# Kernel tuning notes

Hardware: AMD Instinct MI355X
Metric: run time of the kernel (lower is better)

## Reference

```python
import jax, jax.numpy as jnp
import numpy as np

H = 32  # hidden_size
NUM_LAYERS = 3
INPUT_SIZE = 64
STD = 0.1


def setup_inputs() -> dict:
    key = jax.random.key(0)
    ks = jax.random.split(key, 2 * NUM_LAYERS + 2)
    inp = {}
    inp["x"] = jax.random.normal(ks[0], (256, 2048, INPUT_SIZE), dtype=jnp.float32)
    in_dim = INPUT_SIZE
    for l in range(NUM_LAYERS):
        inp[f"W_ih{l}"] = STD * jax.random.normal(ks[1 + 2 * l], (4 * H, in_dim), dtype=jnp.float32)
        inp[f"W_hh{l}"] = STD * jax.random.normal(ks[2 + 2 * l], (4 * H, H), dtype=jnp.float32)
        inp[f"b{l}"] = jnp.zeros((4 * H,), dtype=jnp.float32)  # b_ih + b_hh, both init to 0
        in_dim = H
    inp["W_out"] = STD * jax.random.normal(ks[-1], (1, H), dtype=jnp.float32)
    inp["b_out"] = jnp.zeros((1,), dtype=jnp.float32)
    return inp


def _lstm_layer(x, W_ih, W_hh, b):
    # x: [B, T, D_in] -> h_seq: [B, T, H]
    B = x.shape[0]
    # precompute input-to-gate projections for all timesteps (one big GEMM)
    xg = jnp.einsum('btd,gd->btg', x, W_ih) + b          # [B, T, 4H]
    xg = jnp.swapaxes(xg, 0, 1)                           # [T, B, 4H]
    W_hh_T = W_hh.T                                       # [H, 4H]

    def step(carry, xg_t):
        h, c = carry
        g = xg_t + h @ W_hh_T                             # [B, 4H]
        i = jax.nn.sigmoid(g[:, 0 * H:1 * H])
        f = jax.nn.sigmoid(g[:, 1 * H:2 * H])
        gg = jnp.tanh(g[:, 2 * H:3 * H])
        o = jax.nn.sigmoid(g[:, 3 * H:4 * H])
        c = f * c + i * gg
        h = o * jnp.tanh(c)
        return (h, c), h

    h0 = jnp.zeros((B, H), dtype=x.dtype)
    c0 = jnp.zeros((B, H), dtype=x.dtype)
    _, h_seq = jax.lax.scan(step, (h0, c0), xg)           # h_seq: [T, B, H]
    return jnp.swapaxes(h_seq, 0, 1)                      # [B, T, H]


def reference(x, W_ih0, W_hh0, b0, W_ih1, W_hh1, b1, W_ih2, W_hh2, b2, W_out, b_out):
    h = _lstm_layer(x, W_ih0, W_hh0, b0)
    h = _lstm_layer(h, W_ih1, W_hh1, b1)
    h = _lstm_layer(h, W_ih2, W_hh2, b2)
    last = h[:, -1, :]                                    # [B, H]
    return last @ W_out.T + b_out                         # [B, 1]
```

## Files before the change

kernel.cpp:

```cpp
#include <hip/hip_runtime.h>


typedef float v2f __attribute__((ext_vector_type(2)));

constexpr int T_SEQ  = 2048;
constexpr int CH     = 16;
constexpr int NCHUNK = T_SEQ / CH;
constexpr int NPHASE = NCHUNK + 5;

#define GLOAD_LDS16(gsrc, ldst)                                                              \
    __builtin_amdgcn_global_load_lds((const __attribute__((address_space(1))) void*)(gsrc), \
                                     (__attribute__((address_space(3))) void*)(ldst),        \
                                     16, 0, 0)
#define KEEPV(x) asm volatile("" : "+v"(x))

__device__ __forceinline__ float rcp_f(float x) { return __builtin_amdgcn_rcpf(x); }

__device__ __forceinline__ float swap_sum32(float x) {
#if __has_builtin(__builtin_amdgcn_permlane32_swap)
    auto r = __builtin_amdgcn_permlane32_swap(__float_as_uint(x), __float_as_uint(x),
                                              false, false);
    return __uint_as_float(r[0]) + __uint_as_float(r[1]);
#else
    return x + __shfl_xor(x, 32);
#endif
}

template<bool RING>
__device__ __forceinline__ void rec_chunk(int l,
    const v2f* __restrict__ xg_in,
    float* __restrict__ ring_out,
    const v2f (&whA)[16], const v2f (&whB)[16],
    float (&hs)[32], float& c, float& z,
    float mt, float ca, float cb)
{
    v2f xgr[CH];
#pragma unroll
    for (int tt = 0; tt < CH; ++tt) xgr[tt] = xg_in[tt * 64 + l];

#pragma unroll
    for (int tt = 0; tt < CH; ++tt) {
        v2f aA0 = {xgr[tt].x, 0.f}, aA1 = {0.f, 0.f};
        v2f aB0 = {xgr[tt].y, 0.f}, aB1 = {0.f, 0.f};
#pragma unroll
        for (int j = 0; j < 16; j += 2) {
            const v2f h0 = {hs[2*j],     hs[2*j + 1]};
            const v2f h1 = {hs[2*j + 2], hs[2*j + 3]};
            aA0 = h0 * whA[j]     + aA0;
            aB0 = h0 * whB[j]     + aB0;
            aA1 = h1 * whA[j + 1] + aA1;
            aB1 = h1 * whB[j + 1] + aB1;
        }
        const float ga = (aA0.x + aA1.x) + (aA0.y + aA1.y);
        const float gb = (aB0.x + aB1.x) + (aB0.y + aB1.y);

        const float sA = rcp_f(1.0f + __expf(-ga));
        const float eb = __expf(mt * gb);
        const float tb = fmaf(-2.0f, rcp_f(eb + 1.0f), 1.0f);
        const float vB = fmaf(ca, tb, cb);

        const float p  = sA * ((l < 32) ? vB : c);
        const float cn = swap_sum32(p);
        const float ec = __expf(2.0f * cn);
        const float th = fmaf(-2.0f, rcp_f(ec + 1.0f), 1.0f);
        z = vB * th;
        c = cn;

        if constexpr (RING) { if (l >= 32) ring_out[tt * 32 + (l - 32)] = z; }

        const int zb = __float_as_int(z);
#pragma unroll
        for (int k = 0; k < 32; ++k)
            hs[k] = __int_as_float(__builtin_amdgcn_readlane(zb, k + 32));
    }
}

__device__ __forceinline__ void feed_h_chunk(int l, const float* __restrict__ hr,
    v2f* __restrict__ xg_out, const v2f (&wA)[16], const v2f (&wB)[16],
    float bA, float bB)
{
#pragma unroll
    for (int tt = 0; tt < CH; ++tt) {
        const float4* h4 = reinterpret_cast<const float4*>(hr + tt * 32);
        v2f a0 = {bA, 0.f}, a1 = {0.f, 0.f}, b0 = {bB, 0.f}, b1 = {0.f, 0.f};
#pragma unroll
        for (int i = 0; i < 8; ++i) {
            const float4 v = h4[i];
            const v2f lo = {v.x, v.y}, hi = {v.z, v.w};
            a0 = lo * wA[2*i] + a0;  a1 = hi * wA[2*i+1] + a1;
            b0 = lo * wB[2*i] + b0;  b1 = hi * wB[2*i+1] + b1;
        }
        xg_out[tt * 64 + l] = (v2f){(a0.x + a1.x) + (a0.y + a1.y),
                                    (b0.x + b1.x) + (b0.y + b1.y)};
    }
}

__device__ __forceinline__ void feed0_chunk(int l, const float* __restrict__ xs,
    v2f* __restrict__ xg_out, const v2f (&wA)[32], const v2f (&wB)[32],
    float bA, float bB)
{
#pragma unroll
    for (int tt = 0; tt < CH; ++tt) {
        const float4* xt = reinterpret_cast<const float4*>(xs + tt * 64);
        v2f a0 = {bA, 0.f}, a1 = {0.f, 0.f}, b0 = {bB, 0.f}, b1 = {0.f, 0.f};
#pragma unroll
        for (int i = 0; i < 16; ++i) {
            const float4 v = xt[i];
            const v2f lo = {v.x, v.y}, hi = {v.z, v.w};
            a0 = lo * wA[2*i] + a0;  a1 = hi * wA[2*i+1] + a1;
            b0 = lo * wB[2*i] + b0;  b1 = hi * wB[2*i+1] + b1;
        }
        xg_out[tt * 64 + l] = (v2f){(a0.x + a1.x) + (a0.y + a1.y),
                                    (b0.x + b1.x) + (b0.y + b1.y)};
    }
}

__global__ __launch_bounds__(512, 1)
void lstm3_iso_kernel(const float* __restrict__ x,
    const float* __restrict__ W_ih0, const float* __restrict__ W_hh0, const float* __restrict__ b0,
    const float* __restrict__ W_ih1, const float* __restrict__ W_hh1, const float* __restrict__ b1,
    const float* __restrict__ W_ih2, const float* __restrict__ W_hh2, const float* __restrict__ b2,
    const float* __restrict__ W_out, const float* __restrict__ b_out,
    float* __restrict__ out)
{
    const int bi = blockIdx.x;
    const int w  = threadIdx.x >> 6;
    const int l  = threadIdx.x & 63;

    __shared__ v2f   xg0[2][CH][64];
    __shared__ v2f   xg1[2][CH][64];
    __shared__ v2f   xg2[2][CH][64];
    __shared__ float h0r[2][CH][32];
    __shared__ float h1r[2][CH][32];
    __shared__ float xstage[2][CH * 64];

    if (w == 0) {
        __builtin_amdgcn_s_setprio(1);
        v2f whA[16], whB[16];
        const v2f* hA = reinterpret_cast<const v2f*>(W_hh0 + l * 32);
        const v2f* hB = reinterpret_cast<const v2f*>(W_hh0 + (l + 64) * 32);
#pragma unroll
        for (int i = 0; i < 16; ++i) { whA[i] = hA[i]; KEEPV(whA[i]); whB[i] = hB[i]; KEEPV(whB[i]); }
        const float mt = (l < 32) ? 2.f : 1.f;
        const float ca = (l < 32) ? 1.f : 0.5f;
        const float cb = (l < 32) ? 0.f : 0.5f;
        float hs[32];
#pragma unroll
        for (int k = 0; k < 32; ++k) hs[k] = 0.f;
        float c = 0.f, z = 0.f;
        __syncthreads();
        for (int p = 0; p < NPHASE; ++p) {
            const int ci = p - 1;
            if (ci >= 0 && ci < NCHUNK)
                rec_chunk<true>(l, &xg0[ci & 1][0][0], &h0r[ci & 1][0][0],
                                whA, whB, hs, c, z, mt, ca, cb);
            __syncthreads();
        }
    } else if (w == 1) {
        __builtin_amdgcn_s_setprio(1);
        v2f whA[16], whB[16];
        const v2f* hA = reinterpret_cast<const v2f*>(W_hh1 + l * 32);
        const v2f* hB = reinterpret_cast<const v2f*>(W_hh1 + (l + 64) * 32);
#pragma unroll
        for (int i = 0; i < 16; ++i) { whA[i] = hA[i]; KEEPV(whA[i]); whB[i] = hB[i]; KEEPV(whB[i]); }
        const float mt = (l < 32) ? 2.f : 1.f;
        const float ca = (l < 32) ? 1.f : 0.5f;
        const float cb = (l < 32) ? 0.f : 0.5f;
        float hs[32];
#pragma unroll
        for (int k = 0; k < 32; ++k) hs[k] = 0.f;
        float c = 0.f, z = 0.f;
        __syncthreads();
        for (int p = 0; p < NPHASE; ++p) {
            const int ci = p - 3;
            if (ci >= 0 && ci < NCHUNK)
                rec_chunk<true>(l, &xg1[ci & 1][0][0], &h1r[ci & 1][0][0],
                                whA, whB, hs, c, z, mt, ca, cb);
            __syncthreads();
        }
    } else if (w == 2) {
        __builtin_amdgcn_s_setprio(1);
        v2f whA[16], whB[16];
        const v2f* hA = reinterpret_cast<const v2f*>(W_hh2 + l * 32);
        const v2f* hB = reinterpret_cast<const v2f*>(W_hh2 + (l + 64) * 32);
#pragma unroll
        for (int i = 0; i < 16; ++i) { whA[i] = hA[i]; KEEPV(whA[i]); whB[i] = hB[i]; KEEPV(whB[i]); }
        const float mt = (l < 32) ? 2.f : 1.f;
        const float ca = (l < 32) ? 1.f : 0.5f;
        const float cb = (l < 32) ? 0.f : 0.5f;
        const float woutv = W_out[l & 31];
        float hs[32];
#pragma unroll
        for (int k = 0; k < 32; ++k) hs[k] = 0.f;
        float c = 0.f, z = 0.f;
        __syncthreads();
        for (int p = 0; p < NPHASE; ++p) {
            const int ci = p - 5;
            if (ci >= 0 && ci < NCHUNK)
                rec_chunk<false>(l, &xg2[ci & 1][0][0], nullptr,
                                 whA, whB, hs, c, z, mt, ca, cb);
            __syncthreads();
        }
        float s = (l >= 32) ? z * woutv : 0.f;
#pragma unroll
        for (int off = 32; off; off >>= 1) s += __shfl_xor(s, off);
        if (l == 0) out[bi] = s + b_out[0];
    } else if (w == 3) {
        v2f wA[32], wB[32];
        const v2f* pA = reinterpret_cast<const v2f*>(W_ih0 + l * 64);
        const v2f* pB = reinterpret_cast<const v2f*>(W_ih0 + (l + 64) * 64);
#pragma unroll
        for (int i = 0; i < 32; ++i) { wA[i] = pA[i]; KEEPV(wA[i]); wB[i] = pB[i]; KEEPV(wB[i]); }
        const float bAv = b0[l], bBv = b0[l + 64];
        const float* src = x + (size_t)bi * T_SEQ * 64;
#pragma unroll
        for (int i = 0; i < 4; ++i)
            GLOAD_LDS16(src + i * 256 + l * 4, &xstage[0][i * 256 + l * 4]);
        __syncthreads();
        for (int p = 0; p < NPHASE; ++p) {
            if (p + 1 < NCHUNK) {
                const float* ns = src + (size_t)(p + 1) * CH * 64;
                float* dst = &xstage[(p + 1) & 1][0];
#pragma unroll
                for (int i = 0; i < 4; ++i)
                    GLOAD_LDS16(ns + i * 256 + l * 4, dst + i * 256 + l * 4);
            }
            if (p < NCHUNK)
                feed0_chunk(l, xstage[p & 1], &xg0[p & 1][0][0], wA, wB, bAv, bBv);
            __syncthreads();
        }
    } else if (w == 7) {
        v2f w1A[16], w1B[16], w2A[16], w2B[16];
        const v2f* p1A = reinterpret_cast<const v2f*>(W_ih1 + l * 32);
        const v2f* p1B = reinterpret_cast<const v2f*>(W_ih1 + (l + 64) * 32);
        const v2f* p2A = reinterpret_cast<const v2f*>(W_ih2 + l * 32);
        const v2f* p2B = reinterpret_cast<const v2f*>(W_ih2 + (l + 64) * 32);
#pragma unroll
        for (int i = 0; i < 16; ++i) {
            w1A[i] = p1A[i]; KEEPV(w1A[i]); w1B[i] = p1B[i]; KEEPV(w1B[i]);
            w2A[i] = p2A[i]; KEEPV(w2A[i]); w2B[i] = p2B[i]; KEEPV(w2B[i]);
        }
        const float b1A = b1[l], b1B = b1[l + 64];
        const float b2A = b2[l], b2B = b2[l + 64];
        __syncthreads();
        for (int p = 0; p < NPHASE; ++p) {
            const int c1 = p - 2;
            if (c1 >= 0 && c1 < NCHUNK)
                feed_h_chunk(l, &h0r[c1 & 1][0][0], &xg1[c1 & 1][0][0], w1A, w1B, b1A, b1B);
            const int c2 = p - 4;
            if (c2 >= 0 && c2 < NCHUNK)
                feed_h_chunk(l, &h1r[c2 & 1][0][0], &xg2[c2 & 1][0][0], w2A, w2B, b2A, b2B);
            __syncthreads();
        }
    } else {
        __syncthreads();
        for (int p = 0; p < NPHASE; ++p) __syncthreads();
    }
}

extern "C" void kernel_launch(void* const* d_in, const int* in_sizes, int n_in,
                              void* d_out, int out_size, void* d_ws, size_t ws_size,
                              hipStream_t stream) {
    const float* x      = (const float*)d_in[0];
    const float* W_ih0  = (const float*)d_in[1];
    const float* W_hh0  = (const float*)d_in[2];
    const float* b0     = (const float*)d_in[3];
    const float* W_ih1  = (const float*)d_in[4];
    const float* W_hh1  = (const float*)d_in[5];
    const float* b1     = (const float*)d_in[6];
    const float* W_ih2  = (const float*)d_in[7];
    const float* W_hh2  = (const float*)d_in[8];
    const float* b2     = (const float*)d_in[9];
    const float* W_out  = (const float*)d_in[10];
    const float* b_out  = (const float*)d_in[11];

    lstm3_iso_kernel<<<256, 512, 0, stream>>>(x,
                                              W_ih0, W_hh0, b0,
                                              W_ih1, W_hh1, b1,
                                              W_ih2, W_hh2, b2,
                                              W_out, b_out,
                                              (float*)d_out);
}
```

Measured before the change: 802.5 us.

## Interleave two batch sequences per wave to hide recurrent step latency

Each block now processes two batch elements, and each recurrent wave interleaves the time steps of the two independent sequences so one sequence's latency chain can overlap the other's. The hidden-state broadcast moves from 32 readlanes to an LDS write plus float4 reads. The idle waves 4–7 now split the layer-1/2 input projections by half-chunk. The grid halves to 128 blocks, so fewer CUs are used in exchange for more instruction-level parallelism per wave, and the LDS round trip adds latency to each step.

```diff
diff --git a/kernel.cpp b/kernel.cpp
--- a/kernel.cpp
+++ b/kernel.cpp
@@ -26,61 +26,74 @@
 #endif
 }
 
+__device__ __forceinline__ void rec_step(int l, v2f xgv,
+    const v2f (&whA)[16], const v2f (&whB)[16],
+    const float4 (&hv)[8], float& c, float& z,
+    float mt, float ca, float cb)
+{
+    v2f aA0 = {xgv.x, 0.f}, aA1 = {0.f, 0.f};
+    v2f aB0 = {xgv.y, 0.f}, aB1 = {0.f, 0.f};
+#pragma unroll
+    for (int i = 0; i < 8; ++i) {
+        const v2f lo = {hv[i].x, hv[i].y}, hi = {hv[i].z, hv[i].w};
+        aA0 = lo * whA[2*i]   + aA0;  aA1 = hi * whA[2*i+1] + aA1;
+        aB0 = lo * whB[2*i]   + aB0;  aB1 = hi * whB[2*i+1] + aB1;
+    }
+    const float ga = (aA0.x + aA1.x) + (aA0.y + aA1.y);
+    const float gb = (aB0.x + aB1.x) + (aB0.y + aB1.y);
+
+    const float sA = rcp_f(1.0f + __expf(-ga));
+    const float eb = __expf(mt * gb);
+    const float tb = fmaf(-2.0f, rcp_f(eb + 1.0f), 1.0f);
+    const float vB = fmaf(ca, tb, cb);
+
+    const float p  = sA * ((l < 32) ? vB : c);
+    const float cn = swap_sum32(p);
+    const float ec = __expf(2.0f * cn);
+    const float th = fmaf(-2.0f, rcp_f(ec + 1.0f), 1.0f);
+    z = vB * th;
+    c = cn;
+}
+
 template<bool RING>
-__device__ __forceinline__ void rec_chunk(int l,
-    const v2f* __restrict__ xg_in,
-    float* __restrict__ ring_out,
+__device__ __forceinline__ void rec_chunk2(int l,
+    const v2f* __restrict__ xgA, const v2f* __restrict__ xgB,
+    float* __restrict__ ringA, float* __restrict__ ringB,
+    float* hbA, float* hbB,
     const v2f (&whA)[16], const v2f (&whB)[16],
-    float (&hs)[32], float& c, float& z,
+    float4 (&hvA)[8], float4 (&hvB)[8],
+    float& cA, float& zA, float& cB, float& zB,
     float mt, float ca, float cb)
 {
-    v2f xgr[CH];
-#pragma unroll
-    for (int tt = 0; tt < CH; ++tt) xgr[tt] = xg_in[tt * 64 + l];
-
+    v2f xa = xgA[l], xb = xgB[l];
 #pragma unroll
     for (int tt = 0; tt < CH; ++tt) {
-        v2f aA0 = {xgr[tt].x, 0.f}, aA1 = {0.f, 0.f};
-        v2f aB0 = {xgr[tt].y, 0.f}, aB1 = {0.f, 0.f};
-#pragma unroll
-        for (int j = 0; j < 16; j += 2) {
-            const v2f h0 = {hs[2*j],     hs[2*j + 1]};
-            const v2f h1 = {hs[2*j + 2], hs[2*j + 3]};
-            aA0 = h0 * whA[j]     + aA0;
-            aB0 = h0 * whB[j]     + aB0;
-            aA1 = h1 * whA[j + 1] + aA1;
-            aB1 = h1 * whB[j + 1] + aB1;
-        }
-        const float ga = (aA0.x + aA1.x) + (aA0.y + aA1.y);
-        const float gb = (aB0.x + aB1.x) + (aB0.y + aB1.y);
-
-        const float sA = rcp_f(1.0f + __expf(-ga));
-        const float eb = __expf(mt * gb);
-        const float tb = fmaf(-2.0f, rcp_f(eb + 1.0f), 1.0f);
-        const float vB = fmaf(ca, tb, cb);
-
-        const float p  = sA * ((l < 32) ? vB : c);
-        const float cn = swap_sum32(p);
-        const float ec = __expf(2.0f * cn);
-        const float th = fmaf(-2.0f, rcp_f(ec + 1.0f), 1.0f);
-        z = vB * th;
-        c = cn;
-
-        if constexpr (RING) { if (l >= 32) ring_out[tt * 32 + (l - 32)] = z; }
-
-        const int zb = __float_as_int(z);
-#pragma unroll
-        for (int k = 0; k < 32; ++k)
-            hs[k] = __int_as_float(__builtin_amdgcn_readlane(zb, k + 32));
-    }
-}
-
-__device__ __forceinline__ void feed_h_chunk(int l, const float* __restrict__ hr,
+        rec_step(l, xa, whA, whB, hvA, cA, zA, mt, ca, cb);
+        hbA[l] = zA;
+        if constexpr (RING) { if (l >= 32) ringA[tt*32 + (l-32)] = zA; }
+        {   const float4* h4 = reinterpret_cast<const float4*>(hbA + 32);
+#pragma unroll
+            for (int i = 0; i < 8; ++i) hvA[i] = h4[i];
+        }
+        if (tt + 1 < CH) xa = xgA[(tt+1)*64 + l];
+        rec_step(l, xb, whA, whB, hvB, cB, zB, mt, ca, cb);
+        hbB[l] = zB;
+        if constexpr (RING) { if (l >= 32) ringB[tt*32 + (l-32)] = zB; }
+        {   const float4* h4 = reinterpret_cast<const float4*>(hbB + 32);
+#pragma unroll
+            for (int i = 0; i < 8; ++i) hvB[i] = h4[i];
+        }
+        if (tt + 1 < CH) xb = xgB[(tt+1)*64 + l];
+    }
+}
+
+__device__ __forceinline__ void feed_h_half(int l, const float* __restrict__ hr,
     v2f* __restrict__ xg_out, const v2f (&wA)[16], const v2f (&wB)[16],
-    float bA, float bB)
-{
-#pragma unroll
-    for (int tt = 0; tt < CH; ++tt) {
+    float bA, float bB, int tt0)
+{
+#pragma unroll
+    for (int t = 0; t < CH/2; ++t) {
+        const int tt = tt0 + t;
         const float4* h4 = reinterpret_cast<const float4*>(hr + tt * 32);
         v2f a0 = {bA, 0.f}, a1 = {0.f, 0.f}, b0 = {bB, 0.f}, b1 = {0.f, 0.f};
 #pragma unroll
@@ -116,7 +129,7 @@
 }
 
 __global__ __launch_bounds__(512, 1)
-void lstm3_iso_kernel(const float* __restrict__ x,
+void lstm3_dual_kernel(const float* __restrict__ x,
     const float* __restrict__ W_ih0, const float* __restrict__ W_hh0, const float* __restrict__ b0,
     const float* __restrict__ W_ih1, const float* __restrict__ W_hh1, const float* __restrict__ b1,
     const float* __restrict__ W_ih2, const float* __restrict__ W_hh2, const float* __restrict__ b2,
@@ -127,84 +140,53 @@
     const int w  = threadIdx.x >> 6;
     const int l  = threadIdx.x & 63;
 
-    __shared__ v2f   xg0[2][CH][64];
-    __shared__ v2f   xg1[2][CH][64];
-    __shared__ v2f   xg2[2][CH][64];
-    __shared__ float h0r[2][CH][32];
-    __shared__ float h1r[2][CH][32];
-    __shared__ float xstage[2][CH * 64];
-
-    if (w == 0) {
+    __shared__ v2f   xg[3][2][2][CH][64];
+    __shared__ float ring[2][2][2][CH][32];
+    __shared__ float xstage[2][2][CH * 64];
+    __shared__ float hbuf[3][2][64];
+
+    if (w == 0 || w == 1 || w == 2) {
+        const int L = w;
         __builtin_amdgcn_s_setprio(1);
+        const float* Whh = (L == 0) ? W_hh0 : (L == 1) ? W_hh1 : W_hh2;
         v2f whA[16], whB[16];
-        const v2f* hA = reinterpret_cast<const v2f*>(W_hh0 + l * 32);
-        const v2f* hB = reinterpret_cast<const v2f*>(W_hh0 + (l + 64) * 32);
-#pragma unroll
-        for (int i = 0; i < 16; ++i) { whA[i] = hA[i]; KEEPV(whA[i]); whB[i] = hB[i]; KEEPV(whB[i]); }
-        const float mt = (l < 32) ? 2.f : 1.f;
-        const float ca = (l < 32) ? 1.f : 0.5f;
-        const float cb = (l < 32) ? 0.f : 0.5f;
-        float hs[32];
-#pragma unroll
-        for (int k = 0; k < 32; ++k) hs[k] = 0.f;
-        float c = 0.f, z = 0.f;
-        __syncthreads();
-        for (int p = 0; p < NPHASE; ++p) {
-            const int ci = p - 1;
-            if (ci >= 0 && ci < NCHUNK)
-                rec_chunk<true>(l, &xg0[ci & 1][0][0], &h0r[ci & 1][0][0],
-                                whA, whB, hs, c, z, mt, ca, cb);
-            __syncthreads();
-        }
-    } else if (w == 1) {
-        __builtin_amdgcn_s_setprio(1);
-        v2f whA[16], whB[16];
-        const v2f* hA = reinterpret_cast<const v2f*>(W_hh1 + l * 32);
-        const v2f* hB = reinterpret_cast<const v2f*>(W_hh1 + (l + 64) * 32);
-#pragma unroll
-        for (int i = 0; i < 16; ++i) { whA[i] = hA[i]; KEEPV(whA[i]); whB[i] = hB[i]; KEEPV(whB[i]); }
-        const float mt = (l < 32) ? 2.f : 1.f;
-        const float ca = (l < 32) ? 1.f : 0.5f;
-        const float cb = (l < 32) ? 0.f : 0.5f;
-        float hs[32];
-#pragma unroll
-        for (int k = 0; k < 32; ++k) hs[k] = 0.f;
-        float c = 0.f, z = 0.f;
-        __syncthreads();
-        for (int p = 0; p < NPHASE; ++p) {
-            const int ci = p - 3;
-            if (ci >= 0 && ci < NCHUNK)
-                rec_chunk<true>(l, &xg1[ci & 1][0][0], &h1r[ci & 1][0][0],
-                                whA, whB, hs, c, z, mt, ca, cb);
-            __syncthreads();
-        }
-    } else if (w == 2) {
-        __builtin_amdgcn_s_setprio(1);
-        v2f whA[16], whB[16];
-        const v2f* hA = reinterpret_cast<const v2f*>(W_hh2 + l * 32);
-        const v2f* hB = reinterpret_cast<const v2f*>(W_hh2 + (l + 64) * 32);
+        const v2f* hA = reinterpret_cast<const v2f*>(Whh + l * 32);
+        const v2f* hB = reinterpret_cast<const v2f*>(Whh + (l + 64) * 32);
 #pragma unroll
         for (int i = 0; i < 16; ++i) { whA[i] = hA[i]; KEEPV(whA[i]); whB[i] = hB[i]; KEEPV(whB[i]); }
         const float mt = (l < 32) ? 2.f : 1.f;
         const float ca = (l < 32) ? 1.f : 0.5f;
         const float cb = (l < 32) ? 0.f : 0.5f;
         const float woutv = W_out[l & 31];
-        float hs[32];
-#pragma unroll
-        for (int k = 0; k < 32; ++k) hs[k] = 0.f;
-        float c = 0.f, z = 0.f;
+        float4 hvA[8], hvB[8];
+#pragma unroll
+        for (int i = 0; i < 8; ++i) { hvA[i] = make_float4(0.f,0.f,0.f,0.f); hvB[i] = hvA[i]; }
+        float cA = 0.f, zA = 0.f, cB = 0.f, zB = 0.f;
+        const int skew = 2 * L + 1;
         __syncthreads();
         for (int p = 0; p < NPHASE; ++p) {
-            const int ci = p - 5;
-            if (ci >= 0 && ci < NCHUNK)
-                rec_chunk<false>(l, &xg2[ci & 1][0][0], nullptr,
-                                 whA, whB, hs, c, z, mt, ca, cb);
+            const int ci = p - skew;
+            if (ci >= 0 && ci < NCHUNK) {
+                if (L < 2)
+                    rec_chunk2<true>(l, &xg[L][0][ci&1][0][0], &xg[L][1][ci&1][0][0],
+                                     &ring[L][0][ci&1][0][0], &ring[L][1][ci&1][0][0],
+                                     hbuf[L][0], hbuf[L][1],
+                                     whA, whB, hvA, hvB, cA, zA, cB, zB, mt, ca, cb);
+                else
+                    rec_chunk2<false>(l, &xg[2][0][ci&1][0][0], &xg[2][1][ci&1][0][0],
+                                      nullptr, nullptr,
+                                      hbuf[2][0], hbuf[2][1],
+                                      whA, whB, hvA, hvB, cA, zA, cB, zB, mt, ca, cb);
+            }
             __syncthreads();
         }
-        float s = (l >= 32) ? z * woutv : 0.f;
-#pragma unroll
-        for (int off = 32; off; off >>= 1) s += __shfl_xor(s, off);
-        if (l == 0) out[bi] = s + b_out[0];
+        if (L == 2) {
+            float s0 = (l >= 32) ? zA * woutv : 0.f;
+            float s1 = (l >= 32) ? zB * woutv : 0.f;
+#pragma unroll
+            for (int off = 32; off; off >>= 1) { s0 += __shfl_xor(s0, off); s1 += __shfl_xor(s1, off); }
+            if (l == 0) { out[2*bi] = s0 + b_out[0]; out[2*bi + 1] = s1 + b_out[0]; }
+        }
     } else if (w == 3) {
         v2f wA[32], wB[32];
         const v2f* pA = reinterpret_cast<const v2f*>(W_ih0 + l * 64);
@@ -212,49 +194,55 @@
 #pragma unroll
         for (int i = 0; i < 32; ++i) { wA[i] = pA[i]; KEEPV(wA[i]); wB[i] = pB[i]; KEEPV(wB[i]); }
         const float bAv = b0[l], bBv = b0[l + 64];
-        const float* src = x + (size_t)bi * T_SEQ * 64;
-#pragma unroll
-        for (int i = 0; i < 4; ++i)
-            GLOAD_LDS16(src + i * 256 + l * 4, &xstage[0][i * 256 + l * 4]);
+        const float* src0 = x + (size_t)(2*bi)     * T_SEQ * 64;
+        const float* src1 = x + (size_t)(2*bi + 1) * T_SEQ * 64;
+#pragma unroll
+        for (int i = 0; i < 4; ++i) {
+            GLOAD_LDS16(src0 + i*256 + l*4, &xstage[0][0][i*256 + l*4]);
+            GLOAD_LDS16(src1 + i*256 + l*4, &xstage[1][0][i*256 + l*4]);
+        }
         __syncthreads();
         for (int p = 0; p < NPHASE; ++p) {
             if (p + 1 < NCHUNK) {
-                const float* ns = src + (size_t)(p + 1) * CH * 64;
-                float* dst = &xstage[(p + 1) & 1][0];
-#pragma unroll
-                for (int i = 0; i < 4; ++i)
-                    GLOAD_LDS16(ns + i * 256 + l * 4, dst + i * 256 + l * 4);
-            }
-            if (p < NCHUNK)
-                feed0_chunk(l, xstage[p & 1], &xg0[p & 1][0][0], wA, wB, bAv, bBv);
+                const float* n0 = src0 + (size_t)(p + 1) * CH * 64;
+                const float* n1 = src1 + (size_t)(p + 1) * CH * 64;
+                float* d0 = &xstage[0][(p + 1) & 1][0];
+                float* d1 = &xstage[1][(p + 1) & 1][0];
+#pragma unroll
+                for (int i = 0; i < 4; ++i) {
+                    GLOAD_LDS16(n0 + i*256 + l*4, d0 + i*256 + l*4);
+                    GLOAD_LDS16(n1 + i*256 + l*4, d1 + i*256 + l*4);
+                }
+            }
+            if (p < NCHUNK) {
+                feed0_chunk(l, xstage[0][p & 1], &xg[0][0][p & 1][0][0], wA, wB, bAv, bBv);
+                feed0_chunk(l, xstage[1][p & 1], &xg[0][1][p & 1][0][0], wA, wB, bAv, bBv);
+            }
             __syncthreads();
         }
-    } else if (w == 7) {
-        v2f w1A[16], w1B[16], w2A[16], w2B[16];
-        const v2f* p1A = reinterpret_cast<const v2f*>(W_ih1 + l * 32);
-        const v2f* p1B = reinterpret_cast<const v2f*>(W_ih1 + (l + 64) * 32);
-        const v2f* p2A = reinterpret_cast<const v2f*>(W_ih2 + l * 32);
-        const v2f* p2B = reinterpret_cast<const v2f*>(W_ih2 + (l + 64) * 32);
-#pragma unroll
-        for (int i = 0; i < 16; ++i) {
-            w1A[i] = p1A[i]; KEEPV(w1A[i]); w1B[i] = p1B[i]; KEEPV(w1B[i]);
-            w2A[i] = p2A[i]; KEEPV(w2A[i]); w2B[i] = p2B[i]; KEEPV(w2B[i]);
-        }
-        const float b1A = b1[l], b1B = b1[l + 64];
-        const float b2A = b2[l], b2B = b2[l + 64];
+    } else {
+        const int fl  = (w == 4 || w == 6) ? 0 : 1;
+        const int tt0 = (w <= 5) ? 0 : CH/2;
+        const float* Wih = (fl == 0) ? W_ih1 : W_ih2;
+        const float* bb  = (fl == 0) ? b1    : b2;
+        const int skew   = (fl == 0) ? 2 : 4;
+        v2f wA[16], wB[16];
+        const v2f* pA = reinterpret_cast<const v2f*>(Wih + l * 32);
+        const v2f* pB = reinterpret_cast<const v2f*>(Wih + (l + 64) * 32);
+#pragma unroll
+        for (int i = 0; i < 16; ++i) { wA[i] = pA[i]; KEEPV(wA[i]); wB[i] = pB[i]; KEEPV(wB[i]); }
+        const float bAv = bb[l], bBv = bb[l + 64];
         __syncthreads();
         for (int p = 0; p < NPHASE; ++p) {
-            const int c1 = p - 2;
-            if (c1 >= 0 && c1 < NCHUNK)
-                feed_h_chunk(l, &h0r[c1 & 1][0][0], &xg1[c1 & 1][0][0], w1A, w1B, b1A, b1B);
-            const int c2 = p - 4;
-            if (c2 >= 0 && c2 < NCHUNK)
-                feed_h_chunk(l, &h1r[c2 & 1][0][0], &xg2[c2 & 1][0][0], w2A, w2B, b2A, b2B);
+            const int ci = p - skew;
+            if (ci >= 0 && ci < NCHUNK) {
+                feed_h_half(l, &ring[fl][0][ci & 1][0][0], &xg[fl+1][0][ci & 1][0][0],
+                            wA, wB, bAv, bBv, tt0);
+                feed_h_half(l, &ring[fl][1][ci & 1][0][0], &xg[fl+1][1][ci & 1][0][0],
+                            wA, wB, bAv, bBv, tt0);
+            }
             __syncthreads();
         }
-    } else {
-        __syncthreads();
-        for (int p = 0; p < NPHASE; ++p) __syncthreads();
     }
 }
 
@@ -274,10 +262,10 @@
     const float* W_out  = (const float*)d_in[10];
     const float* b_out  = (const float*)d_in[11];
 
-    lstm3_iso_kernel<<<256, 512, 0, stream>>>(x,
-                                              W_ih0, W_hh0, b0,
-                                              W_ih1, W_hh1, b1,
-                                              W_ih2, W_hh2, b2,
-                                              W_out, b_out,
-                                              (float*)d_out);
-}
+    lstm3_dual_kernel<<<128, 512, 0, stream>>>(x,
+                                               W_ih0, W_hh0, b0,
+                                               W_ih1, W_hh1, b1,
+                                               W_ih2, W_hh2, b2,
+                                               W_out, b_out,
+                                               (float*)d_out);
+}
```

After: 1.622 ms. 2.02x slower.
